# Performance work log

Hardware: AMD Instinct MI355X
Metric: run time of the kernel (lower is better)

The kernel has to match this reference:

```python
import jax, jax.numpy as jnp
import numpy as np

CHUNK = 256
THETA = 10000.0

def rope2d(x):
    # x: (b, h, n, d), d divisible by 4
    b, h, n, d = x.shape
    pad = (-n) % CHUNK
    if pad:
        x = jnp.pad(x, ((0, 0), (0, 0), (0, pad), (0, 0)))
    c = (n + pad) // CHUNK
    x = x.reshape(b, h, c, CHUNK, d)
    inv = 1.0 / THETA ** (jnp.arange(0, d, 4, dtype=jnp.float32) / d)  # (d/4,)
    fl = jnp.arange(CHUNK, dtype=jnp.float32)[:, None] * inv[None, :]  # (l, d/4)
    cos_l, sin_l = jnp.cos(fl), jnp.sin(fl)
    fc = jnp.arange(c, dtype=jnp.float32)[:, None] * inv[None, :]      # (c, d/4)
    cos_c, sin_c = jnp.cos(fc)[:, None, :], jnp.sin(fc)[:, None, :]    # (c, 1, d/4)
    x1, x2, x3, x4 = jnp.split(x, 4, axis=-1)
    r1 = x1 * cos_l - x2 * sin_l
    r2 = x1 * sin_l + x2 * cos_l
    r3 = x3 * cos_c - x4 * sin_c
    r4 = x3 * sin_c + x4 * cos_c
    out = jnp.concatenate([r1, r2, r3, r4], axis=-1).reshape(b, h, c * CHUNK, d)
    return out[:, :, :n]


def setup_inputs():
    key = jax.random.key(0)
    ks = jax.random.split(key, 6)
    dim, heads = 512, 8
    b, n = 2, 2048
    s = 0.02
    return {
        'x': jax.random.normal(ks[0], (b, n, dim), dtype=jnp.float32),
        'w_qkv': jax.random.normal(ks[1], (3 * dim, dim), dtype=jnp.float32) * s,
        'b_qkv': jnp.zeros((3 * dim,), dtype=jnp.float32),
        'w_pre': jax.random.normal(ks[2], (heads, heads), dtype=jnp.float32) * 0.3,
        'w_post': jax.random.normal(ks[3], (heads, heads), dtype=jnp.float32) * 0.3,
        'w_out': jax.random.normal(ks[4], (dim, dim), dtype=jnp.float32) * s,
        'b_out': jnp.zeros((dim,), dtype=jnp.float32),
    }


def reference(x, w_qkv, b_qkv, w_pre, w_post, w_out, b_out):
    b, n, dim = x.shape
    heads = w_pre.shape[0]
    d = dim // heads
    scale = d ** -0.5
    qkv = x @ w_qkv.T + b_qkv                      # (b, n, 3*dim)
    q, k, v = jnp.split(qkv, 3, axis=-1)
    def to_heads(t):
        return t.reshape(b, n, heads, d).transpose(0, 2, 1, 3)  # (b, h, n, d)
    q, k, v = to_heads(q), to_heads(k), to_heads(v)
    q = rope2d(q)
    k = rope2d(k)
    logits = jnp.einsum('bhid,bhjd->bhij', q, k) * scale
    # talking-heads pre-softmax mix (Linear over head dim, no bias)
    logits = jnp.einsum('bhij,gh->bgij', logits, w_pre)
    attn = jax.nn.softmax(logits, axis=-1)
    # post-softmax mix
    attn = jnp.einsum('bhij,gh->bgij', attn, w_post)
    out = jnp.einsum('bhij,bhjd->bhid', attn, v)   # (b, h, n, d)
    out = out.transpose(0, 2, 1, 3).reshape(b, n, dim)
    return out @ w_out.T + b_out
```

## Files before the change

kernel.cpp:

```cpp
#include <hip/hip_runtime.h>
#include <hip/hip_bf16.h>

typedef __attribute__((ext_vector_type(8))) short bf16x8;
typedef __attribute__((ext_vector_type(4))) float f32x4;

#define DEV static __device__ __forceinline__

DEV unsigned short f2bf(float f) {
    union { float f; unsigned int u; } v; v.f = f;
    return (unsigned short)((v.u + 0x7FFFu + ((v.u >> 16) & 1u)) >> 16);
}
DEV float bf2f(unsigned short s) {
    union { unsigned int u; float f; } v; v.u = ((unsigned int)s) << 16; return v.f;
}
DEV bf16x8 ld_bf8(const unsigned short* p) {
    return *reinterpret_cast<const bf16x8*>(p);
}
DEV f32x4 mfma16(bf16x8 a, bf16x8 b, f32x4 c) {
    return __builtin_amdgcn_mfma_f32_16x16x32_bf16(a, b, c, 0, 0, 0);
}
DEV bf16x8 make_wfrag(const float* wmat, int li, int lg, float scale) {
    bf16x8 f = {};
    if (lg == 0 && li < 8) {
        #pragma unroll
        for (int t = 0; t < 8; t++) f[t] = (short)f2bf(wmat[li*8 + t] * scale);
    }
    return f;
}

__global__ void k_cvt(const float* __restrict__ s, unsigned short* __restrict__ d, int n) {
    int i = (blockIdx.x * blockDim.x + threadIdx.x) * 4;
    if (i >= n) return;
    float4 v = *reinterpret_cast<const float4*>(s + i);
    ushort4 o = { f2bf(v.x), f2bf(v.y), f2bf(v.z), f2bf(v.w) };
    *reinterpret_cast<ushort4*>(d + i) = o;
}

__global__ __launch_bounds__(256) void k_qkv(
    const unsigned short* __restrict__ xb, const unsigned short* __restrict__ wb,
    const float* __restrict__ bias,
    unsigned short* __restrict__ Qb, unsigned short* __restrict__ Kb,
    unsigned short* __restrict__ Vt)
{
    __shared__ unsigned short As[64][40];
    __shared__ unsigned short Bs[64][40];
    const int m0 = blockIdx.x * 64, c0 = blockIdx.y * 64;
    const int t = threadIdx.x;
    const int w = t >> 6, lane = t & 63, li = lane & 15, lg = lane >> 4;
    const int wr = w >> 1, wc = w & 1;
    f32x4 acc[2][2] = {};
    const int srow = t >> 2, spart = (t & 3) * 8;
    for (int kt = 0; kt < 512; kt += 32) {
        *reinterpret_cast<uint4*>(&As[srow][spart]) =
            *reinterpret_cast<const uint4*>(&xb[(size_t)(m0 + srow) * 512 + kt + spart]);
        *reinterpret_cast<uint4*>(&Bs[srow][spart]) =
            *reinterpret_cast<const uint4*>(&wb[(size_t)(c0 + srow) * 512 + kt + spart]);
        __syncthreads();
        bf16x8 af[2], bfr[2];
        #pragma unroll
        for (int mf = 0; mf < 2; mf++) af[mf] = ld_bf8(&As[wr*32 + mf*16 + li][lg*8]);
        #pragma unroll
        for (int nf = 0; nf < 2; nf++) bfr[nf] = ld_bf8(&Bs[wc*32 + nf*16 + li][lg*8]);
        #pragma unroll
        for (int mf = 0; mf < 2; mf++)
            #pragma unroll
            for (int nf = 0; nf < 2; nf++)
                acc[mf][nf] = mfma16(af[mf], bfr[nf], acc[mf][nf]);
        __syncthreads();
    }
    const int type = c0 >> 9;
    const int head = (c0 & 511) >> 6;
    const float b0 = bias[c0 + wc*32 + li];
    const float b1 = bias[c0 + wc*32 + 16 + li];
    float invf = 0.f;
    if (type < 2) invf = powf(10000.f, -(float)li * (1.f/16.f));
    #pragma unroll
    for (int mf = 0; mf < 2; mf++) {
        #pragma unroll
        for (int r = 0; r < 4; r++) {
            int grow = m0 + wr*32 + mf*16 + lg*4 + r;
            int tok = grow & 2047, bb = grow >> 11;
            float v0 = acc[mf][0][r] + b0;
            float v1 = acc[mf][1][r] + b1;
            if (type < 2) {
                float ang = (wc == 0 ? (float)(tok & 255) : (float)(tok >> 8)) * invf;
                float s, c;
                sincosf(ang, &s, &c);
                float r0 = v0 * c - v1 * s;
                float r1 = v0 * s + v1 * c;
                unsigned short* dst = (type == 0 ? Qb : Kb);
                size_t base = (((size_t)(bb*8 + head)) * 2048 + tok) * 64 + wc*32 + li;
                dst[base]      = f2bf(r0);
                dst[base + 16] = f2bf(r1);
            } else {
                size_t base = (((size_t)(bb*8 + head)) * 64 + wc*32 + li) * 2048 + tok;
                Vt[base]             = f2bf(v0);
                Vt[base + 16 * 2048] = f2bf(v1);
            }
        }
    }
}

__global__ __launch_bounds__(512, 4) void k_lsum(
    const unsigned short* __restrict__ Qb, const unsigned short* __restrict__ Kb,
    const float* __restrict__ w_pre, float* __restrict__ Lp)
{
    __shared__ unsigned short Lt[8192];
    const int orig = blockIdx.x;
    const int virt = ((orig & 7) << 6) | (orig >> 3);
    const int jh = virt & 1, it = (virt >> 1) & 127, bb = virt >> 8;
    const int i0 = it * 16;
    const int tid = threadIdx.x, w = tid >> 6, lane = tid & 63, li = lane & 15, lg = lane >> 4;
    bf16x8 W1f = make_wfrag(w_pre, li, lg, 0.125f * 1.44269504088896340736f);
    const unsigned short* Qp = Qb + (((size_t)(bb*8 + w)) * 2048 + i0 + li) * 64;
    bf16x8 qa0 = ld_bf8(Qp + lg*8), qa1 = ld_bf8(Qp + 32 + lg*8);
    const unsigned short* Kp = Kb + ((size_t)(bb*8 + w)) * 2048 * 64;
    const f32x4 zero = {};
    float lacc0 = 0.f, lacc1 = 0.f;
    #pragma unroll 1
    for (int t = 0; t < 16; t++) {
        const int j0 = jh*1024 + t*64;
        f32x4 sa[4] = {};
        #pragma unroll
        for (int nf = 0; nf < 4; nf++) {
            const unsigned short* kp = Kp + (size_t)(j0 + nf*16 + li) * 64;
            sa[nf] = mfma16(qa0, ld_bf8(kp + lg*8), sa[nf]);
            sa[nf] = mfma16(qa1, ld_bf8(kp + 32 + lg*8), sa[nf]);
        }
        __syncthreads();
        #pragma unroll
        for (int nf = 0; nf < 4; nf++)
            #pragma unroll
            for (int r = 0; r < 4; r++)
                Lt[((lg*4 + r)*64 + nf*16 + li)*8 + w] = f2bf(sa[nf][r]);
        __syncthreads();
        #pragma unroll
        for (int x = 0; x < 2; x++) {
            const int i = 2*w + x;
            float s = 0.f;
            #pragma unroll
            for (int jj = 0; jj < 4; jj++) {
                const int e0 = i*64 + jj*16;
                bf16x8 bfv = {};
                if (lg == 0) bfv = *(const bf16x8*)&Lt[(e0 + li)*8];
                f32x4 d = mfma16(bfv, W1f, zero);
                s += (exp2f(d[0]) + exp2f(d[1])) + (exp2f(d[2]) + exp2f(d[3]));
            }
            if (x == 0) lacc0 += s; else lacc1 += s;
        }
    }
    lacc0 += __shfl_xor(lacc0, 16); lacc0 += __shfl_xor(lacc0, 32);
    lacc1 += __shfl_xor(lacc1, 16); lacc1 += __shfl_xor(lacc1, 32);
    if (lg == 0 && li < 8) {
        float* Lpw = Lp + (size_t)jh * 32768;
        size_t base = (size_t)bb*2048 + i0;
        Lpw[(base + 2*w + 0)*8 + li] = lacc0;
        Lpw[(base + 2*w + 1)*8 + li] = lacc1;
    }
}

__global__ __launch_bounds__(512, 4) void k_attn(
    const unsigned short* __restrict__ Qb, const unsigned short* __restrict__ Kb,
    const unsigned short* __restrict__ Vt,
    const float* __restrict__ w_pre, const float* __restrict__ w_post,
    const float* __restrict__ Lp,
    unsigned short* __restrict__ AOp0, unsigned short* __restrict__ AOp1)
{
    __shared__ unsigned short Lt[8192];
    __shared__ unsigned short Ah[8 * 1168];
    __shared__ float Llds[128];
    const int orig = blockIdx.x;
    const int virt = ((orig & 7) << 6) | (orig >> 3);
    const int jh = virt & 1, it = (virt >> 1) & 127, bb = virt >> 8;
    const int i0 = it * 16;
    const int tid = threadIdx.x, w = tid >> 6, lane = tid & 63, li = lane & 15, lg = lane >> 4;
    bf16x8 W1f = make_wfrag(w_pre, li, lg, 0.125f * 1.44269504088896340736f);
    bf16x8 W2f = make_wfrag(w_post, li, lg, 1.0f);
    if (tid < 128) {
        size_t g = ((size_t)bb*2048 + i0 + (tid >> 3)) * 8 + (tid & 7);
        Llds[tid] = 1.0f / (Lp[g] + Lp[32768 + g]);
    }
    const unsigned short* Qp = Qb + (((size_t)(bb*8 + w)) * 2048 + i0 + li) * 64;
    bf16x8 qa0 = ld_bf8(Qp + lg*8), qa1 = ld_bf8(Qp + 32 + lg*8);
    const unsigned short* Kp = Kb + ((size_t)(bb*8 + w)) * 2048 * 64;
    const unsigned short* Vp = Vt + ((size_t)(bb*8 + w)) * 64 * 2048;
    __syncthreads();
    const int lgc = lg & 1;
    f32x4 invlA = *(const f32x4*)&Llds[(2*w + 0)*8 + lgc*4];
    f32x4 invlB = *(const f32x4*)&Llds[(2*w + 1)*8 + lgc*4];
    const f32x4 zero = {};
    f32x4 oacc[4] = {};
    #pragma unroll 1
    for (int t = 0; t < 16; t++) {
        const int j0 = jh*1024 + t*64;
        bf16x8 vf[8];
        #pragma unroll
        for (int nf = 0; nf < 4; nf++) {
            const unsigned short* vp = Vp + (size_t)(nf*16 + li) * 2048 + j0;
            vf[nf*2]   = ld_bf8(vp + lg*8);
            vf[nf*2+1] = ld_bf8(vp + 32 + lg*8);
        }
        f32x4 sa[4] = {};
        #pragma unroll
        for (int nf = 0; nf < 4; nf++) {
            const unsigned short* kp = Kp + (size_t)(j0 + nf*16 + li) * 64;
            sa[nf] = mfma16(qa0, ld_bf8(kp + lg*8), sa[nf]);
            sa[nf] = mfma16(qa1, ld_bf8(kp + 32 + lg*8), sa[nf]);
        }
        #pragma unroll
        for (int nf = 0; nf < 4; nf++)
            #pragma unroll
            for (int r = 0; r < 4; r++)
                Lt[((lg*4 + r)*64 + nf*16 + li)*8 + w] = f2bf(sa[nf][r]);
        __syncthreads();
        #pragma unroll
        for (int x = 0; x < 2; x++) {
            const int i = 2*w + x;
            f32x4 invl = x ? invlB : invlA;
            #pragma unroll
            for (int jj = 0; jj < 4; jj++) {
                const int e0 = i*64 + jj*16;
                bf16x8 bfv = {};
                if (lg == 0) bfv = *(const bf16x8*)&Lt[(e0 + li)*8];
                f32x4 d = mfma16(W1f, bfv, zero);
                float p0 = exp2f(d[0]) * invl[0];
                float p1 = exp2f(d[1]) * invl[1];
                float p2 = exp2f(d[2]) * invl[2];
                float p3 = exp2f(d[3]) * invl[3];
                unsigned lo = (unsigned)f2bf(p0) | ((unsigned)f2bf(p1) << 16);
                unsigned hi = (unsigned)f2bf(p2) | ((unsigned)f2bf(p3) << 16);
                unsigned plo = (unsigned)__shfl_xor((int)lo, 16);
                unsigned phi = (unsigned)__shfl_xor((int)hi, 16);
                union { unsigned u[4]; bf16x8 v; } af;
                af.u[0] = lo; af.u[1] = hi; af.u[2] = plo; af.u[3] = phi;
                f32x4 a2 = mfma16(af.v, W2f, zero);
                if (li < 8) {
                    ushort4 o = { f2bf(a2[0]), f2bf(a2[1]), f2bf(a2[2]), f2bf(a2[3]) };
                    *(ushort4*)&Ah[li*1168 + i*72 + jj*16 + lg*4] = o;
                }
            }
        }
        __syncthreads();
        #pragma unroll
        for (int kk = 0; kk < 2; kk++) {
            bf16x8 pa = *(const bf16x8*)&Ah[w*1168 + li*72 + kk*32 + lg*8];
            #pragma unroll
            for (int nf = 0; nf < 4; nf++)
                oacc[nf] = mfma16(pa, vf[nf*2 + kk], oacc[nf]);
        }
    }
    unsigned short* ao = jh ? AOp1 : AOp0;
    #pragma unroll
    for (int nf = 0; nf < 4; nf++)
        #pragma unroll
        for (int r = 0; r < 4; r++)
            ao[((size_t)bb*2048 + i0 + lg*4 + r)*512 + w*64 + nf*16 + li] = f2bf(oacc[nf][r]);
}

__global__ __launch_bounds__(256) void k_out(
    const unsigned short* __restrict__ a0, const unsigned short* __restrict__ a1,
    const unsigned short* __restrict__ wb, const float* __restrict__ bias,
    float* __restrict__ out)
{
    __shared__ unsigned short As[64][40];
    __shared__ unsigned short Bs[64][40];
    const int m0 = blockIdx.x * 64, c0 = blockIdx.y * 64;
    const int t = threadIdx.x;
    const int w = t >> 6, lane = t & 63, li = lane & 15, lg = lane >> 4;
    const int wr = w >> 1, wc = w & 1;
    f32x4 acc[2][2] = {};
    const int srow = t >> 2, spart = (t & 3) * 8;
    for (int kt = 0; kt < 512; kt += 32) {
        size_t aidx = (size_t)(m0 + srow) * 512 + kt + spart;
        uint4 ua = *(const uint4*)&a0[aidx];
        uint4 ub = *(const uint4*)&a1[aidx];
        const unsigned short* pa = (const unsigned short*)&ua;
        const unsigned short* pb = (const unsigned short*)&ub;
        unsigned short us[8];
        #pragma unroll
        for (int q = 0; q < 8; q++) us[q] = f2bf(bf2f(pa[q]) + bf2f(pb[q]));
        *reinterpret_cast<uint4*>(&As[srow][spart]) = *(const uint4*)us;
        *reinterpret_cast<uint4*>(&Bs[srow][spart]) =
            *reinterpret_cast<const uint4*>(&wb[(size_t)(c0 + srow) * 512 + kt + spart]);
        __syncthreads();
        bf16x8 af[2], bfr[2];
        #pragma unroll
        for (int mf = 0; mf < 2; mf++) af[mf] = ld_bf8(&As[wr*32 + mf*16 + li][lg*8]);
        #pragma unroll
        for (int nf = 0; nf < 2; nf++) bfr[nf] = ld_bf8(&Bs[wc*32 + nf*16 + li][lg*8]);
        #pragma unroll
        for (int mf = 0; mf < 2; mf++)
            #pragma unroll
            for (int nf = 0; nf < 2; nf++)
                acc[mf][nf] = mfma16(af[mf], bfr[nf], acc[mf][nf]);
        __syncthreads();
    }
    #pragma unroll
    for (int mf = 0; mf < 2; mf++)
        #pragma unroll
        for (int nf = 0; nf < 2; nf++)
            #pragma unroll
            for (int r = 0; r < 4; r++) {
                int grow = m0 + wr*32 + mf*16 + lg*4 + r;
                int gcol = c0 + wc*32 + nf*16 + li;
                out[(size_t)grow * 512 + gcol] = acc[mf][nf][r] + bias[gcol];
            }
}

extern "C" void kernel_launch(void* const* d_in, const int* in_sizes, int n_in,
                              void* d_out, int out_size, void* d_ws, size_t ws_size,
                              hipStream_t stream)
{
    const float* x      = (const float*)d_in[0];
    const float* w_qkv  = (const float*)d_in[1];
    const float* b_qkv  = (const float*)d_in[2];
    const float* w_pre  = (const float*)d_in[3];
    const float* w_post = (const float*)d_in[4];
    const float* w_out  = (const float*)d_in[5];
    const float* b_out  = (const float*)d_in[6];
    float* out = (float*)d_out;

    char* ws = (char*)d_ws;
    unsigned short* xb    = (unsigned short*)(ws);
    unsigned short* AOp1  = (unsigned short*)(ws);
    unsigned short* wqkvb = (unsigned short*)(ws + 4194304);
    unsigned short* woutb = (unsigned short*)(ws + 5767168);
    unsigned short* Qb    = (unsigned short*)(ws + 6291456);
    unsigned short* Kb    = (unsigned short*)(ws + 10485760);
    unsigned short* Vt    = (unsigned short*)(ws + 14680064);
    unsigned short* AOp0  = (unsigned short*)(ws + 18874368);
    float* Lp             = (float*)(ws + 23068672);

    k_cvt<<<2048, 256, 0, stream>>>(x, xb, 2097152);
    k_cvt<<<768, 256, 0, stream>>>(w_qkv, wqkvb, 786432);
    k_cvt<<<256, 256, 0, stream>>>(w_out, woutb, 262144);
    k_qkv<<<dim3(64, 24), 256, 0, stream>>>(xb, wqkvb, b_qkv, Qb, Kb, Vt);
    k_lsum<<<512, 512, 0, stream>>>(Qb, Kb, w_pre, Lp);
    k_attn<<<512, 512, 0, stream>>>(Qb, Kb, Vt, w_pre, w_post, Lp, AOp0, AOp1);
    k_out<<<dim3(64, 8), 256, 0, stream>>>(AOp0, AOp1, woutb, b_out, out);
}
```

Baseline: 251.0 us.

## Fuse fp32-to-bf16 conversion into GEMMs and software-pipeline attention loops

Drops the three separate conversion kernels. The QKV and output GEMMs now load fp32 and convert to bf16 while staging tiles into shared memory, which saves launches and a round trip through global memory, but the GEMMs read twice the bytes. The k_lsum and k_attn loops are software-pipelined with double-buffered logit tiles (LtA/LtB) and register prefetch of the next K/V fragments, so the QK MFMAs for one tile overlap the mixing, softmax and PV work of the previous one. This raises register and LDS use, which may reduce occupancy. f2bf also switches to the HIP intrinsic conversion.

```diff
diff --git a/kernel.cpp b/kernel.cpp
--- a/kernel.cpp
+++ b/kernel.cpp
@@ -7,15 +7,13 @@
 #define DEV static __device__ __forceinline__
 
 DEV unsigned short f2bf(float f) {
-    union { float f; unsigned int u; } v; v.f = f;
-    return (unsigned short)((v.u + 0x7FFFu + ((v.u >> 16) & 1u)) >> 16);
+    __hip_bfloat16 h = __float2bfloat16(f);
+    return __builtin_bit_cast(unsigned short, h);
 }
 DEV float bf2f(unsigned short s) {
     union { unsigned int u; float f; } v; v.u = ((unsigned int)s) << 16; return v.f;
 }
-DEV bf16x8 ld_bf8(const unsigned short* p) {
-    return *reinterpret_cast<const bf16x8*>(p);
-}
+DEV bf16x8 ld_bf8(const unsigned short* p) { return *reinterpret_cast<const bf16x8*>(p); }
 DEV f32x4 mfma16(bf16x8 a, bf16x8 b, f32x4 c) {
     return __builtin_amdgcn_mfma_f32_16x16x32_bf16(a, b, c, 0, 0, 0);
 }
@@ -28,16 +26,8 @@
     return f;
 }
 
-__global__ void k_cvt(const float* __restrict__ s, unsigned short* __restrict__ d, int n) {
-    int i = (blockIdx.x * blockDim.x + threadIdx.x) * 4;
-    if (i >= n) return;
-    float4 v = *reinterpret_cast<const float4*>(s + i);
-    ushort4 o = { f2bf(v.x), f2bf(v.y), f2bf(v.z), f2bf(v.w) };
-    *reinterpret_cast<ushort4*>(d + i) = o;
-}
-
 __global__ __launch_bounds__(256) void k_qkv(
-    const unsigned short* __restrict__ xb, const unsigned short* __restrict__ wb,
+    const float* __restrict__ xf, const float* __restrict__ wf,
     const float* __restrict__ bias,
     unsigned short* __restrict__ Qb, unsigned short* __restrict__ Kb,
     unsigned short* __restrict__ Vt)
@@ -51,10 +41,16 @@
     f32x4 acc[2][2] = {};
     const int srow = t >> 2, spart = (t & 3) * 8;
     for (int kt = 0; kt < 512; kt += 32) {
-        *reinterpret_cast<uint4*>(&As[srow][spart]) =
-            *reinterpret_cast<const uint4*>(&xb[(size_t)(m0 + srow) * 512 + kt + spart]);
-        *reinterpret_cast<uint4*>(&Bs[srow][spart]) =
-            *reinterpret_cast<const uint4*>(&wb[(size_t)(c0 + srow) * 512 + kt + spart]);
+        const float* xs = &xf[(size_t)(m0 + srow) * 512 + kt + spart];
+        float4 a0 = *(const float4*)xs, a1 = *(const float4*)(xs + 4);
+        const float* wsrc = &wf[(size_t)(c0 + srow) * 512 + kt + spart];
+        float4 b0 = *(const float4*)wsrc, b1 = *(const float4*)(wsrc + 4);
+        ushort4 ua0 = { f2bf(a0.x), f2bf(a0.y), f2bf(a0.z), f2bf(a0.w) };
+        ushort4 ua1 = { f2bf(a1.x), f2bf(a1.y), f2bf(a1.z), f2bf(a1.w) };
+        ushort4 ub0 = { f2bf(b0.x), f2bf(b0.y), f2bf(b0.z), f2bf(b0.w) };
+        ushort4 ub1 = { f2bf(b1.x), f2bf(b1.y), f2bf(b1.z), f2bf(b1.w) };
+        *(ushort4*)&As[srow][spart] = ua0; *(ushort4*)&As[srow][spart + 4] = ua1;
+        *(ushort4*)&Bs[srow][spart] = ub0; *(ushort4*)&Bs[srow][spart + 4] = ub1;
         __syncthreads();
         bf16x8 af[2], bfr[2];
         #pragma unroll
@@ -70,8 +66,8 @@
     }
     const int type = c0 >> 9;
     const int head = (c0 & 511) >> 6;
-    const float b0 = bias[c0 + wc*32 + li];
-    const float b1 = bias[c0 + wc*32 + 16 + li];
+    const float b0s = bias[c0 + wc*32 + li];
+    const float b1s = bias[c0 + wc*32 + 16 + li];
     float invf = 0.f;
     if (type < 2) invf = powf(10000.f, -(float)li * (1.f/16.f));
     #pragma unroll
@@ -80,8 +76,8 @@
         for (int r = 0; r < 4; r++) {
             int grow = m0 + wr*32 + mf*16 + lg*4 + r;
             int tok = grow & 2047, bb = grow >> 11;
-            float v0 = acc[mf][0][r] + b0;
-            float v1 = acc[mf][1][r] + b1;
+            float v0 = acc[mf][0][r] + b0s;
+            float v1 = acc[mf][1][r] + b1s;
             if (type < 2) {
                 float ang = (wc == 0 ? (float)(tok & 255) : (float)(tok >> 8)) * invf;
                 float s, c;
@@ -101,11 +97,85 @@
     }
 }
 
+#define JC(x) (jh*1024 + ((x) > 15 ? 15 : (x))*64)
+
+#define LOADK(JX) do { const int j0_ = (JX); \
+    _Pragma("unroll") for (int nf = 0; nf < 4; nf++) { \
+        const unsigned short* kp_ = Kp + (size_t)(j0_ + nf*16 + li) * 64; \
+        kf[nf*2]   = ld_bf8(kp_ + lg*8); \
+        kf[nf*2+1] = ld_bf8(kp_ + 32 + lg*8); } \
+} while (0)
+
+#define LOADV(JX) do { const int j0_ = (JX); \
+    _Pragma("unroll") for (int nf = 0; nf < 4; nf++) { \
+        const unsigned short* vp_ = Vp + (size_t)(nf*16 + li) * 2048 + j0_; \
+        vf[nf*2]   = ld_bf8(vp_ + lg*8); \
+        vf[nf*2+1] = ld_bf8(vp_ + 32 + lg*8); } \
+} while (0)
+
+#define QKW(LTW) do { \
+    f32x4 sq0 = {}, sq1 = {}, sq2 = {}, sq3 = {}; \
+    sq0 = mfma16(qa0, kf[0], sq0); sq0 = mfma16(qa1, kf[1], sq0); \
+    sq1 = mfma16(qa0, kf[2], sq1); sq1 = mfma16(qa1, kf[3], sq1); \
+    sq2 = mfma16(qa0, kf[4], sq2); sq2 = mfma16(qa1, kf[5], sq2); \
+    sq3 = mfma16(qa0, kf[6], sq3); sq3 = mfma16(qa1, kf[7], sq3); \
+    _Pragma("unroll") for (int r = 0; r < 4; r++) { \
+        LTW[((lg*4 + r)*64 +  0 + li)*8 + w] = f2bf(sq0[r]); \
+        LTW[((lg*4 + r)*64 + 16 + li)*8 + w] = f2bf(sq1[r]); \
+        LTW[((lg*4 + r)*64 + 32 + li)*8 + w] = f2bf(sq2[r]); \
+        LTW[((lg*4 + r)*64 + 48 + li)*8 + w] = f2bf(sq3[r]); } \
+} while (0)
+
+#define MIX(LTR) do { \
+    _Pragma("unroll") for (int x = 0; x < 2; x++) { \
+        const int i2 = 2*w + x; f32x4 invl = x ? invlB : invlA; \
+        _Pragma("unroll") for (int jj = 0; jj < 4; jj++) { \
+            const int e0 = i2*64 + jj*16; \
+            bf16x8 bfv = {}; \
+            if (lg == 0) bfv = *(const bf16x8*)&LTR[(e0 + li)*8]; \
+            f32x4 d = mfma16(W1f, bfv, zero); \
+            float p0 = exp2f(d[0]) * invl[0], p1 = exp2f(d[1]) * invl[1]; \
+            float p2 = exp2f(d[2]) * invl[2], p3 = exp2f(d[3]) * invl[3]; \
+            unsigned lo = (unsigned)f2bf(p0) | ((unsigned)f2bf(p1) << 16); \
+            unsigned hi = (unsigned)f2bf(p2) | ((unsigned)f2bf(p3) << 16); \
+            unsigned plo = (unsigned)__shfl_xor((int)lo, 16); \
+            unsigned phi = (unsigned)__shfl_xor((int)hi, 16); \
+            union { unsigned u[4]; bf16x8 v; } af_; \
+            af_.u[0] = lo; af_.u[1] = hi; af_.u[2] = plo; af_.u[3] = phi; \
+            f32x4 a2 = mfma16(af_.v, W2f, zero); \
+            if (li < 8) { \
+                ushort4 o = { f2bf(a2[0]), f2bf(a2[1]), f2bf(a2[2]), f2bf(a2[3]) }; \
+                *(ushort4*)&Ah[li*1168 + i2*72 + jj*16 + lg*4] = o; } \
+        } } \
+} while (0)
+
+#define PVOP() do { \
+    _Pragma("unroll") for (int kk = 0; kk < 2; kk++) { \
+        bf16x8 pa = *(const bf16x8*)&Ah[w*1168 + li*72 + kk*32 + lg*8]; \
+        oacc[0] = mfma16(pa, vf[0 + kk], oacc[0]); \
+        oacc[1] = mfma16(pa, vf[2 + kk], oacc[1]); \
+        oacc[2] = mfma16(pa, vf[4 + kk], oacc[2]); \
+        oacc[3] = mfma16(pa, vf[6 + kk], oacc[3]); } \
+} while (0)
+
+#define SUMEXP(LTR) do { \
+    _Pragma("unroll") for (int x = 0; x < 2; x++) { \
+        const int i2 = 2*w + x; float s_ = 0.f; \
+        _Pragma("unroll") for (int jj = 0; jj < 4; jj++) { \
+            const int e0 = i2*64 + jj*16; \
+            bf16x8 bfv = {}; \
+            if (lg == 0) bfv = *(const bf16x8*)&LTR[(e0 + li)*8]; \
+            f32x4 d = mfma16(bfv, W1f, zero); \
+            s_ += (exp2f(d[0]) + exp2f(d[1])) + (exp2f(d[2]) + exp2f(d[3])); } \
+        if (x == 0) lacc0 += s_; else lacc1 += s_; } \
+} while (0)
+
 __global__ __launch_bounds__(512, 4) void k_lsum(
     const unsigned short* __restrict__ Qb, const unsigned short* __restrict__ Kb,
     const float* __restrict__ w_pre, float* __restrict__ Lp)
 {
-    __shared__ unsigned short Lt[8192];
+    __shared__ unsigned short LtA[8192];
+    __shared__ unsigned short LtB[8192];
     const int orig = blockIdx.x;
     const int virt = ((orig & 7) << 6) | (orig >> 3);
     const int jh = virt & 1, it = (virt >> 1) & 127, bb = virt >> 8;
@@ -116,38 +186,22 @@
     bf16x8 qa0 = ld_bf8(Qp + lg*8), qa1 = ld_bf8(Qp + 32 + lg*8);
     const unsigned short* Kp = Kb + ((size_t)(bb*8 + w)) * 2048 * 64;
     const f32x4 zero = {};
+    bf16x8 kf[8];
+    LOADK(JC(0));
+    QKW(LtA);
+    LOADK(JC(1));
+    __syncthreads();
     float lacc0 = 0.f, lacc1 = 0.f;
     #pragma unroll 1
-    for (int t = 0; t < 16; t++) {
-        const int j0 = jh*1024 + t*64;
-        f32x4 sa[4] = {};
-        #pragma unroll
-        for (int nf = 0; nf < 4; nf++) {
-            const unsigned short* kp = Kp + (size_t)(j0 + nf*16 + li) * 64;
-            sa[nf] = mfma16(qa0, ld_bf8(kp + lg*8), sa[nf]);
-            sa[nf] = mfma16(qa1, ld_bf8(kp + 32 + lg*8), sa[nf]);
-        }
-        __syncthreads();
-        #pragma unroll
-        for (int nf = 0; nf < 4; nf++)
-            #pragma unroll
-            for (int r = 0; r < 4; r++)
-                Lt[((lg*4 + r)*64 + nf*16 + li)*8 + w] = f2bf(sa[nf][r]);
-        __syncthreads();
-        #pragma unroll
-        for (int x = 0; x < 2; x++) {
-            const int i = 2*w + x;
-            float s = 0.f;
-            #pragma unroll
-            for (int jj = 0; jj < 4; jj++) {
-                const int e0 = i*64 + jj*16;
-                bf16x8 bfv = {};
-                if (lg == 0) bfv = *(const bf16x8*)&Lt[(e0 + li)*8];
-                f32x4 d = mfma16(bfv, W1f, zero);
-                s += (exp2f(d[0]) + exp2f(d[1])) + (exp2f(d[2]) + exp2f(d[3]));
-            }
-            if (x == 0) lacc0 += s; else lacc1 += s;
-        }
+    for (int tt = 0; tt < 8; tt++) {
+        QKW(LtB);
+        SUMEXP(LtA);
+        LOADK(JC(2*tt + 2));
+        __syncthreads();
+        if (tt < 7) { QKW(LtA); }
+        SUMEXP(LtB);
+        if (tt < 7) { LOADK(JC(2*tt + 3)); }
+        __syncthreads();
     }
     lacc0 += __shfl_xor(lacc0, 16); lacc0 += __shfl_xor(lacc0, 32);
     lacc1 += __shfl_xor(lacc1, 16); lacc1 += __shfl_xor(lacc1, 32);
@@ -166,7 +220,8 @@
     const float* __restrict__ Lp,
     unsigned short* __restrict__ AOp0, unsigned short* __restrict__ AOp1)
 {
-    __shared__ unsigned short Lt[8192];
+    __shared__ unsigned short LtA[8192];
+    __shared__ unsigned short LtB[8192];
     __shared__ unsigned short Ah[8 * 1168];
     __shared__ float Llds[128];
     const int orig = blockIdx.x;
@@ -184,70 +239,32 @@
     bf16x8 qa0 = ld_bf8(Qp + lg*8), qa1 = ld_bf8(Qp + 32 + lg*8);
     const unsigned short* Kp = Kb + ((size_t)(bb*8 + w)) * 2048 * 64;
     const unsigned short* Vp = Vt + ((size_t)(bb*8 + w)) * 64 * 2048;
+    const f32x4 zero = {};
+    bf16x8 kf[8], vf[8];
+    LOADK(JC(0));
+    LOADV(JC(0));
+    QKW(LtA);
+    LOADK(JC(1));
     __syncthreads();
     const int lgc = lg & 1;
     f32x4 invlA = *(const f32x4*)&Llds[(2*w + 0)*8 + lgc*4];
     f32x4 invlB = *(const f32x4*)&Llds[(2*w + 1)*8 + lgc*4];
-    const f32x4 zero = {};
     f32x4 oacc[4] = {};
     #pragma unroll 1
-    for (int t = 0; t < 16; t++) {
-        const int j0 = jh*1024 + t*64;
-        bf16x8 vf[8];
-        #pragma unroll
-        for (int nf = 0; nf < 4; nf++) {
-            const unsigned short* vp = Vp + (size_t)(nf*16 + li) * 2048 + j0;
-            vf[nf*2]   = ld_bf8(vp + lg*8);
-            vf[nf*2+1] = ld_bf8(vp + 32 + lg*8);
-        }
-        f32x4 sa[4] = {};
-        #pragma unroll
-        for (int nf = 0; nf < 4; nf++) {
-            const unsigned short* kp = Kp + (size_t)(j0 + nf*16 + li) * 64;
-            sa[nf] = mfma16(qa0, ld_bf8(kp + lg*8), sa[nf]);
-            sa[nf] = mfma16(qa1, ld_bf8(kp + 32 + lg*8), sa[nf]);
-        }
-        #pragma unroll
-        for (int nf = 0; nf < 4; nf++)
-            #pragma unroll
-            for (int r = 0; r < 4; r++)
-                Lt[((lg*4 + r)*64 + nf*16 + li)*8 + w] = f2bf(sa[nf][r]);
-        __syncthreads();
-        #pragma unroll
-        for (int x = 0; x < 2; x++) {
-            const int i = 2*w + x;
-            f32x4 invl = x ? invlB : invlA;
-            #pragma unroll
-            for (int jj = 0; jj < 4; jj++) {
-                const int e0 = i*64 + jj*16;
-                bf16x8 bfv = {};
-                if (lg == 0) bfv = *(const bf16x8*)&Lt[(e0 + li)*8];
-                f32x4 d = mfma16(W1f, bfv, zero);
-                float p0 = exp2f(d[0]) * invl[0];
-                float p1 = exp2f(d[1]) * invl[1];
-                float p2 = exp2f(d[2]) * invl[2];
-                float p3 = exp2f(d[3]) * invl[3];
-                unsigned lo = (unsigned)f2bf(p0) | ((unsigned)f2bf(p1) << 16);
-                unsigned hi = (unsigned)f2bf(p2) | ((unsigned)f2bf(p3) << 16);
-                unsigned plo = (unsigned)__shfl_xor((int)lo, 16);
-                unsigned phi = (unsigned)__shfl_xor((int)hi, 16);
-                union { unsigned u[4]; bf16x8 v; } af;
-                af.u[0] = lo; af.u[1] = hi; af.u[2] = plo; af.u[3] = phi;
-                f32x4 a2 = mfma16(af.v, W2f, zero);
-                if (li < 8) {
-                    ushort4 o = { f2bf(a2[0]), f2bf(a2[1]), f2bf(a2[2]), f2bf(a2[3]) };
-                    *(ushort4*)&Ah[li*1168 + i*72 + jj*16 + lg*4] = o;
-                }
-            }
-        }
-        __syncthreads();
-        #pragma unroll
-        for (int kk = 0; kk < 2; kk++) {
-            bf16x8 pa = *(const bf16x8*)&Ah[w*1168 + li*72 + kk*32 + lg*8];
-            #pragma unroll
-            for (int nf = 0; nf < 4; nf++)
-                oacc[nf] = mfma16(pa, vf[nf*2 + kk], oacc[nf]);
-        }
+    for (int tt = 0; tt < 8; tt++) {
+        QKW(LtB);
+        MIX(LtA);
+        __syncthreads();
+        PVOP();
+        LOADV(JC(2*tt + 1));
+        LOADK(JC(2*tt + 2));
+        __syncthreads();
+        if (tt < 7) { QKW(LtA); }
+        MIX(LtB);
+        __syncthreads();
+        PVOP();
+        if (tt < 7) { LOADV(JC(2*tt + 2)); LOADK(JC(2*tt + 3)); }
+        __syncthreads();
     }
     unsigned short* ao = jh ? AOp1 : AOp0;
     #pragma unroll
@@ -259,7 +276,7 @@
 
 __global__ __launch_bounds__(256) void k_out(
     const unsigned short* __restrict__ a0, const unsigned short* __restrict__ a1,
-    const unsigned short* __restrict__ wb, const float* __restrict__ bias,
+    const float* __restrict__ wf, const float* __restrict__ bias,
     float* __restrict__ out)
 {
     __shared__ unsigned short As[64][40];
@@ -280,8 +297,11 @@
         #pragma unroll
         for (int q = 0; q < 8; q++) us[q] = f2bf(bf2f(pa[q]) + bf2f(pb[q]));
         *reinterpret_cast<uint4*>(&As[srow][spart]) = *(const uint4*)us;
-        *reinterpret_cast<uint4*>(&Bs[srow][spart]) =
-            *reinterpret_cast<const uint4*>(&wb[(size_t)(c0 + srow) * 512 + kt + spart]);
+        const float* wsrc = &wf[(size_t)(c0 + srow) * 512 + kt + spart];
+        float4 b0 = *(const float4*)wsrc, b1 = *(const float4*)(wsrc + 4);
+        ushort4 ub0 = { f2bf(b0.x), f2bf(b0.y), f2bf(b0.z), f2bf(b0.w) };
+        ushort4 ub1 = { f2bf(b1.x), f2bf(b1.y), f2bf(b1.z), f2bf(b1.w) };
+        *(ushort4*)&Bs[srow][spart] = ub0; *(ushort4*)&Bs[srow][spart + 4] = ub1;
         __syncthreads();
         bf16x8 af[2], bfr[2];
         #pragma unroll
@@ -321,21 +341,15 @@
     float* out = (float*)d_out;
 
     char* ws = (char*)d_ws;
-    unsigned short* xb    = (unsigned short*)(ws);
-    unsigned short* AOp1  = (unsigned short*)(ws);
-    unsigned short* wqkvb = (unsigned short*)(ws + 4194304);
-    unsigned short* woutb = (unsigned short*)(ws + 5767168);
-    unsigned short* Qb    = (unsigned short*)(ws + 6291456);
-    unsigned short* Kb    = (unsigned short*)(ws + 10485760);
-    unsigned short* Vt    = (unsigned short*)(ws + 14680064);
-    unsigned short* AOp0  = (unsigned short*)(ws + 18874368);
-    float* Lp             = (float*)(ws + 23068672);
-
-    k_cvt<<<2048, 256, 0, stream>>>(x, xb, 2097152);
-    k_cvt<<<768, 256, 0, stream>>>(w_qkv, wqkvb, 786432);
-    k_cvt<<<256, 256, 0, stream>>>(w_out, woutb, 262144);
-    k_qkv<<<dim3(64, 24), 256, 0, stream>>>(xb, wqkvb, b_qkv, Qb, Kb, Vt);
+    unsigned short* Qb   = (unsigned short*)(ws);
+    unsigned short* Kb   = (unsigned short*)(ws + 4194304);
+    unsigned short* Vt   = (unsigned short*)(ws + 8388608);
+    unsigned short* AOp0 = (unsigned short*)(ws + 12582912);
+    unsigned short* AOp1 = (unsigned short*)(ws + 16777216);
+    float* Lp            = (float*)(ws + 20971520);
+
+    k_qkv<<<dim3(64, 24), 256, 0, stream>>>(x, w_qkv, b_qkv, Qb, Kb, Vt);
     k_lsum<<<512, 512, 0, stream>>>(Qb, Kb, w_pre, Lp);
     k_attn<<<512, 512, 0, stream>>>(Qb, Kb, Vt, w_pre, w_post, Lp, AOp0, AOp1);
-    k_out<<<dim3(64, 8), 256, 0, stream>>>(AOp0, AOp1, woutb, b_out, out);
-}
+    k_out<<<dim3(64, 8), 256, 0, stream>>>(AOp0, AOp1, w_out, b_out, out);
+}
```

After: 271.3 us. 1.08x slower.
